# Kernel tuning notes

Measured on AMD Instinct MI355X. Metric: run time of the kernel, lower is better.

The kernel has to match this reference:

```python
import jax, jax.numpy as jnp
import numpy as np

B, D = 64, 11                 # trees, tree depth
T = 2 ** D - 1                # 2047 nodes per perfect binary tree (heap layout)
H, E, L, V = 256, 256, 5, 50000
LEAF_START = 2 ** (D - 1) - 1 # first leaf index within a tree
N = B * T


def setup_inputs() -> dict:
    key = jax.random.key(0)
    ks = jax.random.split(key, 8)
    wordid = jax.random.randint(ks[0], (N, L), 0, V, dtype=jnp.int32)
    # subtoken mask: 1 for leaf nodes (which carry tokens), 0 for internal nodes
    node_is_leaf = (jnp.arange(T) >= LEAF_START).astype(jnp.int32)      # [T]
    mask = jnp.tile(node_is_leaf[:, None], (B, L))                       # [N, L]
    h0 = jnp.zeros((N, H), jnp.float32)   # init_hidden -> zeros
    c0 = jnp.zeros((N, H), jnp.float32)
    list_root_index = jnp.zeros((B,), jnp.int32)          # root at offset 0 per tree
    list_num_node = jnp.full((B,), T, dtype=jnp.int32)
    s = 0.02
    emb_table = s * jax.random.normal(ks[1], (V, E), jnp.float32)
    W_iou = s * jax.random.normal(ks[2], (3 * H, E), jnp.float32)
    U_iou = s * jax.random.normal(ks[3], (3 * H, 2 * H), jnp.float32)
    b_iou = jnp.zeros((3 * H,), jnp.float32)
    U_f_w = s * jax.random.normal(ks[4], (2 * H, 2 * H), jnp.float32)
    U_f_b = jnp.zeros((2 * H,), jnp.float32)
    return {"wordid": wordid, "mask": mask, "h0": h0, "c0": c0,
            "list_root_index": list_root_index, "list_num_node": list_num_node,
            "emb_table": emb_table, "W_iou": W_iou, "U_iou": U_iou,
            "b_iou": b_iou, "U_f_w": U_f_w, "U_f_b": U_f_b}


def reference(wordid, mask, h0, c0, list_root_index, list_num_node,
              emb_table, W_iou, U_iou, b_iou, U_f_w, U_f_b):
    fm = mask.astype(jnp.float32)
    # tree_leaf_subtoken path: embed masked ids (masked slots hit token 0, as in torch)
    emb = emb_table[wordid * mask]                # [N, L, E]
    wemb = emb.sum(axis=1)                        # [N, E]
    leaf = fm.max(axis=1)                         # [N] node-level mask
    iou0 = (wemb @ W_iou.T) * leaf[:, None]       # [N, 3H] leaf input contribution
    iou0 = iou0.reshape(B, T, 3 * H)
    c0r = c0.reshape(B, T, H)

    def apply_node(iou, c_in):
        i, o, u = jnp.split(iou + b_iou, 3, axis=-1)
        cn = jax.nn.sigmoid(i) * jnp.tanh(u) + c_in
        return jax.nn.sigmoid(o) * jnp.tanh(cn), cn

    h = jnp.zeros((B, T, H), jnp.float32)
    c = jnp.zeros((B, T, H), jnp.float32)

    # frontier 0: leaves (no in-edges -> reduce never fires, c stays c0)
    hl, cl = apply_node(iou0[:, LEAF_START:], c0r[:, LEAF_START:])
    h = h.at[:, LEAF_START:].set(hl)
    c = c.at[:, LEAF_START:].set(cl)

    # topological propagation, level by level bottom-up
    for d in range(D - 2, -1, -1):
        s, e = 2 ** d - 1, 2 ** (d + 1) - 1
        n = e - s
        # children of nodes [s,e) are contiguous at [e, e+2n) as pairs (2i+1, 2i+2)
        h_cat = h[:, e:e + 2 * n].reshape(B, n, 2 * H)
        f = jax.nn.sigmoid(h_cat @ U_f_w.T + U_f_b).reshape(B, n, 2, H)
        c_red = (f * c[:, e:e + 2 * n].reshape(B, n, 2, H)).sum(axis=2)
        iou = h_cat @ U_iou.T                     # reduce_func REPLACES iou (DGL semantics)
        hn, cn = apply_node(iou, c_red)
        h = h.at[:, s:e].set(hn)
        c = c.at[:, s:e].set(cn)

    # all trees have T nodes -> padded tree_output is just h
    tree_output = h                               # [B, T, H]
    root_h, root_c = h[:, 0], c[:, 0]             # list_root_index == 0
    return tree_output, (root_h, root_c)
```

## Files before the change

### kernel.cpp

```cpp
#include <hip/hip_runtime.h>
#include <math.h>

typedef long long i64;
typedef short short8v __attribute__((ext_vector_type(8)));
typedef float float4v __attribute__((ext_vector_type(4)));

#define Hd 256
#define Bb 64
#define Tn 2047
#define LEAF0 1023
#define NTH 33538048LL

__device__ __forceinline__ float frcp(float x){ return __builtin_amdgcn_rcpf(x); }
__device__ __forceinline__ float sigm(float x){ return frcp(1.0f+__expf(-x)); }
__device__ __forceinline__ float ftanh(float x){ return 1.0f - 2.0f*frcp(__expf(2.0f*x)+1.0f); }
__device__ __forceinline__ float bf2f(unsigned short s){
  union { unsigned u; float f; } v; v.u = ((unsigned)s)<<16; return v.f; }
__device__ __forceinline__ short f2bf(float f){
  union { float f; unsigned u; } v; v.f = f;
  unsigned r = v.u + 0x7FFF + ((v.u>>16)&1);
  return (short)(r>>16); }

#define GL2LDS(gp, lp) __builtin_amdgcn_global_load_lds( \
  (const __attribute__((address_space(1))) void*)(gp), \
  (__attribute__((address_space(3))) void*)(lp), 16, 0, 0)

__global__ __launch_bounds__(256)
void wt2_kernel(const float* __restrict__ W_iou, const float* __restrict__ U_iou,
                const float* __restrict__ U_f_w,
                short* __restrict__ Wt2I, short* __restrict__ Wt2L){
  int t = blockIdx.x*256 + threadIdx.x;
  if (blockIdx.x < 320){
    int lane = t & 63, rest = t >> 6;
    int nr = rest % 20; int rest2 = rest / 20;
    int kt = rest2 & 15, hhb = rest2 >> 4;
    int g = nr/5, strip = nr - g*5;
    int j = strip*256 + hhb*64 + g*16 + (lane&15);
    int k0 = kt*32 + (lane>>4)*8;
    const float* src = (j < 768) ? (U_iou + (i64)j*512 + k0)
                                 : (U_f_w + (i64)(j-768)*512 + k0);
    short* dst = Wt2I + (i64)t*8;
    #pragma unroll
    for (int e=0;e<8;e++) dst[e] = f2bf(src[e]);
  } else {
    int t2 = t - 320*256;
    int lane = t2 & 63, rest = t2 >> 6;
    int nr = rest % 12; int rest2 = rest / 12;
    int kt = rest2 & 7, hhb = rest2 >> 3;
    int g = nr/3, strip = nr - g*3;
    int j = strip*256 + hhb*64 + g*16 + (lane&15);
    int k0 = kt*32 + (lane>>4)*8;
    const float* src = W_iou + (i64)j*256 + k0;
    short* dst = Wt2L + (i64)t2*8;
    #pragma unroll
    for (int e=0;e<8;e++) dst[e] = f2bf(src[e]);
  }
}

__global__ __launch_bounds__(256)
void wemb_kernel(const int* __restrict__ wordid, const float* __restrict__ emb,
                 short* __restrict__ hb, short* __restrict__ cbb){
  int id = blockIdx.x*256 + threadIdx.x;
  int row = id >> 5, q = id & 31;
  int b = row >> 10, j = row & 1023;
  i64 tb = (i64)b*Tn;
  const int* wid = wordid + (tb + LEAF0 + j)*5;
  float s[8];
  #pragma unroll
  for (int e=0;e<8;e++) s[e] = 0.f;
  #pragma unroll
  for (int l=0;l<5;l++){
    const float* er = emb + (i64)wid[l]*Hd + q*8;
    float4 v0 = *(const float4*)(er);
    float4 v1 = *(const float4*)(er+4);
    s[0]+=v0.x; s[1]+=v0.y; s[2]+=v0.z; s[3]+=v0.w;
    s[4]+=v1.x; s[5]+=v1.y; s[6]+=v1.z; s[7]+=v1.w;
  }
  short o[8];
  #pragma unroll
  for (int e=0;e<8;e++) o[e] = f2bf(s[e]);
  short* dst = (j < 1023) ? (hb + (tb + j)*Hd) : (cbb + tb*Hd);
  *(short8v*)(dst + q*8) = *(short8v*)o;
}

#define LEAF_ITER(KT, VM, BU, BL)                                            \
  {                                                                          \
    if ((KT)+2 < 8){                                                         \
      const short* bp = wbB + (i64)((KT)+2)*12*512;                          \
      _Pragma("unroll")                                                      \
      for (int s=0;s<3;s++) BL[s] = *(const short8v*)(bp + (i64)s*512);      \
    }                                                                        \
    asm volatile("" ::: "memory");                                           \
    if ((KT)+3 < 8) GL2LDS(srcA + ((KT)+3)*32, &As[((KT)+3)%5][w*512]);      \
    asm volatile("s_waitcnt vmcnt(" #VM ")" ::: "memory");                   \
    __builtin_amdgcn_s_barrier();                                            \
    asm volatile("" ::: "memory");                                           \
    short8v afr[4];                                                          \
    _Pragma("unroll")                                                        \
    for (int mr=0;mr<4;mr++)                                                 \
      afr[mr] = *(const short8v*)&As[(KT)%5][(wm*4+mr)*512 + lane*8];        \
    _Pragma("unroll")                                                        \
    for (int mr=0;mr<4;mr++)                                                 \
      _Pragma("unroll")                                                      \
      for (int s=0;s<3;s++)                                                  \
        acc[mr][s] = __builtin_amdgcn_mfma_f32_16x16x32_bf16(afr[mr], BU[s], acc[mr][s], 0, 0, 0); \
    asm volatile("s_waitcnt lgkmcnt(0)" ::: "memory");                       \
  }

__global__ __launch_bounds__(512)
void leaf_gemm(const short* __restrict__ hb, const short* __restrict__ cbb,
               const short* __restrict__ WB,
               const float* __restrict__ b_iou, const float* __restrict__ c0,
               float* __restrict__ hOut, short* __restrict__ hbOut,
               short* __restrict__ cbbOut){
  __shared__ __align__(16) short As[5][8*512];
  const int tid = threadIdx.x;
  const int lane = tid & 63, w = tid >> 6;
  const int wm = w >> 2, wg = w & 3;
  const int m0 = blockIdx.x*128;
  const int hhb = blockIdx.y;

  const int rA = m0 + w*16 + (lane&15);
  const int bA = rA >> 10, jA = rA & 1023;
  const short* baseA = (jA < 1023) ? (hb + ((i64)bA*Tn + jA)*Hd)
                                   : (cbb + (i64)bA*Tn*Hd);
  const short* srcA = baseA + (lane>>4)*8;
  const short* wbB = WB + (i64)hhb*96*512 + (i64)(wg*3)*512 + lane*8;

  float4v acc[4][3];
  #pragma unroll
  for (int mr=0;mr<4;mr++)
    #pragma unroll
    for (int s=0;s<3;s++){ float4v z = {0.f,0.f,0.f,0.f}; acc[mr][s] = z; }

  short8v b0[3], b1[3], b2[3];
  #pragma unroll
  for (int s=0;s<3;s++) b0[s] = *(const short8v*)(wbB + (i64)s*512);
  asm volatile("" ::: "memory");
  GL2LDS(srcA, &As[0][w*512]);
  GL2LDS(srcA + 32, &As[1][w*512]);
  GL2LDS(srcA + 64, &As[2][w*512]);
  asm volatile("" ::: "memory");
  #pragma unroll
  for (int s=0;s<3;s++) b1[s] = *(const short8v*)(wbB + (i64)(12+s)*512);
  asm volatile("" ::: "memory");

  LEAF_ITER(0,9,b0,b2)  LEAF_ITER(1,8,b1,b0)
  LEAF_ITER(2,9,b2,b1)  LEAF_ITER(3,9,b0,b2)
  LEAF_ITER(4,9,b1,b0)  LEAF_ITER(5,8,b2,b1)
  LEAF_ITER(6,4,b0,b2)  LEAF_ITER(7,0,b1,b0)

  const int hcol = hhb*64 + wg*16 + (lane&15);
  const float bi = b_iou[hcol], bo = b_iou[256+hcol], bu = b_iou[512+hcol];
  #pragma unroll
  for (int mr=0;mr<4;mr++){
    const int mgb = m0 + wm*64 + mr*16 + ((lane>>4)<<2);
    #pragma unroll
    for (int r=0;r<4;r++){
      const int m = mgb + r;
      const int b = m >> 10, j = m & 1023;
      const i64 n = (i64)b*Tn + LEAF0 + j;
      const float i_ = acc[mr][0][r] + bi;
      const float o_ = acc[mr][1][r] + bo;
      const float u_ = acc[mr][2][r] + bu;
      const float cn = sigm(i_)*ftanh(u_) + c0[n*Hd + hcol];
      const float hv = sigm(o_)*ftanh(cn);
      cbbOut[n*Hd + hcol] = f2bf(cn);
      hbOut[n*Hd + hcol]  = f2bf(hv);
      hOut[n*Hd + hcol] = hv;
    }
  }
}

#define LVL_ITER(KT, VM, BU, BL)                                             \
  {                                                                          \
    if ((KT)+2 < 16){                                                        \
      const short* bp = wbB + (i64)((KT)+2)*20*512;                          \
      _Pragma("unroll")                                                      \
      for (int s=0;s<5;s++) BL[s] = *(const short8v*)(bp + (i64)s*512);      \
    }                                                                        \
    asm volatile("" ::: "memory");                                           \
    if ((KT)+3 < 16) GL2LDS(srcA + ((KT)+3)*32, &As[((KT)+3)%5][w*512]);     \
    asm volatile("s_waitcnt vmcnt(" #VM ")" ::: "memory");                   \
    __builtin_amdgcn_s_barrier();                                            \
    asm volatile("" ::: "memory");                                           \
    short8v afr[4];                                                          \
    _Pragma("unroll")                                                        \
    for (int mr=0;mr<4;mr++)                                                 \
      afr[mr] = *(const short8v*)&As[(KT)%5][(wm*4+mr)*512 + lane*8];        \
    _Pragma("unroll")                                                        \
    for (int mr=0;mr<4;mr++)                                                 \
      _Pragma("unroll")                                                      \
      for (int s=0;s<5;s++)                                                  \
        acc[mr][s] = __builtin_amdgcn_mfma_f32_16x16x32_bf16(afr[mr], BU[s], acc[mr][s], 0, 0, 0); \
    asm volatile("s_waitcnt lgkmcnt(0)" ::: "memory");                       \
  }

__global__ __launch_bounds__(512)
void level_gemm(const short* __restrict__ WB,
                const float* __restrict__ b_iou, const float* __restrict__ U_f_b,
                float* __restrict__ hOut, short* __restrict__ hb, short* __restrict__ cbb,
                int s0, int e0, int logn){
  __shared__ __align__(16) short As[5][8*512];
  const int tid = threadIdx.x;
  const int lane = tid & 63, w = tid >> 6;
  const int wm = w >> 2, wg = w & 3;
  const int m0 = blockIdx.x*128;
  const int hhb = blockIdx.y;
  const int nm1 = (1<<logn)-1;

  const int rA = m0 + w*16 + (lane&15);
  const int bA = rA >> logn, jA = rA & nm1;
  const short* srcA = hb + ((i64)bA*Tn + e0)*Hd + (i64)jA*512 + (lane>>4)*8;
  const short* wbB = WB + (i64)hhb*320*512 + (i64)(wg*5)*512 + lane*8;

  float4v acc[4][5];
  #pragma unroll
  for (int mr=0;mr<4;mr++)
    #pragma unroll
    for (int s=0;s<5;s++){ float4v z = {0.f,0.f,0.f,0.f}; acc[mr][s] = z; }

  short8v b0[5], b1[5], b2[5];
  #pragma unroll
  for (int s=0;s<5;s++) b0[s] = *(const short8v*)(wbB + (i64)s*512);
  asm volatile("" ::: "memory");
  GL2LDS(srcA, &As[0][w*512]);
  GL2LDS(srcA + 32, &As[1][w*512]);
  GL2LDS(srcA + 64, &As[2][w*512]);
  asm volatile("" ::: "memory");
  #pragma unroll
  for (int s=0;s<5;s++) b1[s] = *(const short8v*)(wbB + (i64)(20+s)*512);
  asm volatile("" ::: "memory");

  LVL_ITER( 0,13,b0,b2)  LVL_ITER( 1,12,b1,b0)  LVL_ITER( 2,13,b2,b1)
  LVL_ITER( 3,13,b0,b2)  LVL_ITER( 4,13,b1,b0)  LVL_ITER( 5,13,b2,b1)
  LVL_ITER( 6,13,b0,b2)  LVL_ITER( 7,13,b1,b0)  LVL_ITER( 8,13,b2,b1)
  LVL_ITER( 9,13,b0,b2)  LVL_ITER(10,13,b1,b0)  LVL_ITER(11,13,b2,b1)
  LVL_ITER(12,13,b0,b2)  LVL_ITER(13,12,b1,b0)  LVL_ITER(14, 6,b2,b1)
  LVL_ITER(15, 0,b0,b2)

  const int hcol = hhb*64 + wg*16 + (lane&15);
  const float bi = b_iou[hcol], bo = b_iou[256+hcol], bu = b_iou[512+hcol];
  const float bfl = U_f_b[hcol], bfr2 = U_f_b[256+hcol];
  #pragma unroll
  for (int mr=0;mr<4;mr++){
    const int mgb = m0 + wm*64 + mr*16 + ((lane>>4)<<2);
    #pragma unroll
    for (int r=0;r<4;r++){
      const int m = mgb + r;
      const int b = m >> logn, j = m & nm1;
      const i64 base = (i64)b*Tn;
      const i64 cidx = (base + e0 + 2*j)*Hd + hcol;
      const float cl = bf2f((unsigned short)cbb[cidx]);
      const float cr = bf2f((unsigned short)cbb[cidx + Hd]);
      const float i_ = acc[mr][0][r]+bi, o_ = acc[mr][1][r]+bo, u_ = acc[mr][2][r]+bu;
      const float fl = acc[mr][3][r]+bfl, fr = acc[mr][4][r]+bfr2;
      const float cn = sigm(i_)*ftanh(u_) + sigm(fl)*cl + sigm(fr)*cr;
      const float hv = sigm(o_)*ftanh(cn);
      const i64 oidx = (base + s0 + j)*Hd + hcol;
      cbb[oidx] = f2bf(cn);
      hb[oidx]  = f2bf(hv);
      hOut[oidx] = hv;
    }
  }
}

__global__ __launch_bounds__(512)
void tree_fused(const short* __restrict__ WB, const float* __restrict__ b_iou,
                const float* __restrict__ U_f_b, float* __restrict__ hOut,
                const short* __restrict__ hb, const short* __restrict__ cbb,
                float* __restrict__ outRoot){
  __shared__ __align__(16) short BUF[192*256];
  short* L0H = BUF;
  short* L0C = BUF + 64*256;
  short* L1H = BUF + 128*256;
  short* L1C = BUF + 160*256;
  const int tid = threadIdx.x;
  const int lane = tid & 63, w = tid >> 6;
  const int wm = w >> 2, wg = w & 3;
  const int b = blockIdx.x;
  const i64 tb = (i64)b*Tn;

  #pragma unroll
  for (int p=0;p<4;p++){
    int idx = p*512 + tid;
    int row = idx >> 5, ch = idx & 31;
    int doff = ((row*256 + ch*8)*2) ^ ((row&7)<<4);
    short8v vh = *(const short8v*)(hb  + (tb + 63 + row)*Hd + ch*8);
    short8v vc = *(const short8v*)(cbb + (tb + 63 + row)*Hd + ch*8);
    *(short8v*)((char*)L0H + doff) = vh;
    *(short8v*)((char*)L0C + doff) = vc;
  }
  __syncthreads();

  short* inH = L0H; short* inC = L0C; short* outH = L1H; short* outC = L1C;

  for (int d = 5; d >= 0; --d){
    const int M = 1<<d, s0 = M-1;
    if (wm == 0 || d == 5){
      const int mg = (d == 5) ? wm*16 : 0;
      int j = mg + (lane&15); if (j > s0) j = s0;
      const int k0b = (lane>>4)*8;
      for (int hhb = 0; hhb < 4; ++hhb){
        float4v acc[5];
        #pragma unroll
        for (int s=0;s<5;s++){ float4v z = {0.f,0.f,0.f,0.f}; acc[s] = z; }
        const short* wbB = WB + (i64)hhb*320*512 + (i64)(wg*5)*512 + lane*8;
        #pragma unroll
        for (int kt=0; kt<16; ++kt){
          const int k0 = kt*32 + k0b;
          const int crow = 2*j + (k0>>8), ccol = k0 & 255;
          const int aoff = ((crow*256 + ccol)*2) ^ ((crow&7)<<4);
          short8v a = *(const short8v*)((const char*)inH + aoff);
          const short* bp = wbB + (i64)kt*20*512;
          #pragma unroll
          for (int s=0;s<5;s++){
            short8v bb = *(const short8v*)(bp + (i64)s*512);
            acc[s] = __builtin_amdgcn_mfma_f32_16x16x32_bf16(a, bb, acc[s], 0, 0, 0);
          }
        }
        const int hcol = hhb*64 + wg*16 + (lane&15);
        const float bi = b_iou[hcol], bo = b_iou[256+hcol], bu = b_iou[512+hcol];
        const float bfl = U_f_b[hcol], bfr2 = U_f_b[256+hcol];
        #pragma unroll
        for (int r=0;r<4;r++){
          const int row = mg + ((lane>>4)<<2) + r;
          if (row < M){
            const int c0r = 2*row, c1r = 2*row+1;
            const float cl = bf2f(*(const unsigned short*)((const char*)inC +
                              (((c0r*256 + hcol)*2) ^ ((c0r&7)<<4))));
            const float cr = bf2f(*(const unsigned short*)((const char*)inC +
                              (((c1r*256 + hcol)*2) ^ ((c1r&7)<<4))));
            const float i_ = acc[0][r]+bi, o_ = acc[1][r]+bo, u_ = acc[2][r]+bu;
            const float fl = acc[3][r]+bfl, fr = acc[4][r]+bfr2;
            const float cn = sigm(i_)*ftanh(u_) + sigm(fl)*cl + sigm(fr)*cr;
            const float hv = sigm(o_)*ftanh(cn);
            const int ooff = ((row*256 + hcol)*2) ^ ((row&7)<<4);
            *(short*)((char*)outH + ooff) = f2bf(hv);
            *(short*)((char*)outC + ooff) = f2bf(cn);
            hOut[(tb + s0 + row)*Hd + hcol] = hv;
            if (d == 0){
              outRoot[b*Hd + hcol] = hv;
              outRoot[Bb*Hd + b*Hd + hcol] = cn;
            }
          }
        }
      }
    }
    __syncthreads();
    short* t;
    t = inH; inH = outH; outH = t;
    t = inC; inC = outC; outC = t;
  }
}

extern "C" void kernel_launch(void* const* d_in, const int* in_sizes, int n_in,
                              void* d_out, int out_size, void* d_ws, size_t ws_size,
                              hipStream_t stream){
  const int*   wordid = (const int*)  d_in[0];
  const float* c0     = (const float*)d_in[3];
  const float* emb    = (const float*)d_in[6];
  const float* W_iou  = (const float*)d_in[7];
  const float* U_iou  = (const float*)d_in[8];
  const float* b_iou  = (const float*)d_in[9];
  const float* U_f_w  = (const float*)d_in[10];
  const float* U_f_b  = (const float*)d_in[11];

  float* hOut    = (float*)d_out;
  float* outRoot = hOut + NTH;
  short* cbb  = (short*)d_ws;
  short* hb   = cbb + NTH;
  short* Wt2I = hb + NTH;
  short* Wt2L = Wt2I + 655360;

  hipLaunchKernelGGL(wt2_kernel, dim3(416), dim3(256), 0, stream,
                     W_iou, U_iou, U_f_w, Wt2I, Wt2L);
  hipLaunchKernelGGL(wemb_kernel, dim3(8192), dim3(256), 0, stream,
                     wordid, emb, hb, cbb);
  hipLaunchKernelGGL(leaf_gemm, dim3(512,4), dim3(512), 0, stream,
                     hb, cbb, Wt2L, b_iou, c0, hOut, hb, cbb);
  for (int d = 9; d >= 6; --d){
    const int n = 1<<d, s = n-1, e = 2*n-1;
    const int bm = (64*n + 127)/128;
    hipLaunchKernelGGL(level_gemm, dim3(bm,4), dim3(512), 0, stream,
                       Wt2I, b_iou, U_f_b, hOut, hb, cbb, s, e, d);
  }
  hipLaunchKernelGGL(tree_fused, dim3(64), dim3(512), 0, stream,
                     Wt2I, b_iou, U_f_b, hOut, hb, cbb, outRoot);
}
```

Before: 400.5 us.

## Replace per-tree fused top-level kernel with per-level GEMM launches; merge prep kernels

Removes the tree_fused kernel, which ran the top six levels with one block per tree, and extends the level_gemm launch loop down to the root. level_gemm gains row clamping and bounds checks for levels smaller than a 128-row tile, and writes the root outputs when it processes the root level. The weight-conversion and embedding-sum kernels are merged into one prep kernel to save a launch. This spreads the small top levels over more CUs in exchange for six extra launches and round trips of h and c through global memory, where tree_fused kept them in LDS.

```diff
diff --git a/kernel.cpp b/kernel.cpp
--- a/kernel.cpp
+++ b/kernel.cpp
@@ -26,11 +26,13 @@
   (__attribute__((address_space(3))) void*)(lp), 16, 0, 0)
 
 __global__ __launch_bounds__(256)
-void wt2_kernel(const float* __restrict__ W_iou, const float* __restrict__ U_iou,
-                const float* __restrict__ U_f_w,
-                short* __restrict__ Wt2I, short* __restrict__ Wt2L){
-  int t = blockIdx.x*256 + threadIdx.x;
+void prep_kernel(const float* __restrict__ W_iou, const float* __restrict__ U_iou,
+                 const float* __restrict__ U_f_w,
+                 short* __restrict__ Wt2I, short* __restrict__ Wt2L,
+                 const int* __restrict__ wordid, const float* __restrict__ emb,
+                 short* __restrict__ hb, short* __restrict__ cbb){
   if (blockIdx.x < 320){
+    int t = blockIdx.x*256 + threadIdx.x;
     int lane = t & 63, rest = t >> 6;
     int nr = rest % 20; int rest2 = rest / 20;
     int kt = rest2 & 15, hhb = rest2 >> 4;
@@ -42,8 +44,8 @@
     short* dst = Wt2I + (i64)t*8;
     #pragma unroll
     for (int e=0;e<8;e++) dst[e] = f2bf(src[e]);
-  } else {
-    int t2 = t - 320*256;
+  } else if (blockIdx.x < 416){
+    int t2 = (blockIdx.x-320)*256 + threadIdx.x;
     int lane = t2 & 63, rest = t2 >> 6;
     int nr = rest % 12; int rest2 = rest / 12;
     int kt = rest2 & 7, hhb = rest2 >> 3;
@@ -54,33 +56,29 @@
     short* dst = Wt2L + (i64)t2*8;
     #pragma unroll
     for (int e=0;e<8;e++) dst[e] = f2bf(src[e]);
-  }
-}
-
-__global__ __launch_bounds__(256)
-void wemb_kernel(const int* __restrict__ wordid, const float* __restrict__ emb,
-                 short* __restrict__ hb, short* __restrict__ cbb){
-  int id = blockIdx.x*256 + threadIdx.x;
-  int row = id >> 5, q = id & 31;
-  int b = row >> 10, j = row & 1023;
-  i64 tb = (i64)b*Tn;
-  const int* wid = wordid + (tb + LEAF0 + j)*5;
-  float s[8];
-  #pragma unroll
-  for (int e=0;e<8;e++) s[e] = 0.f;
-  #pragma unroll
-  for (int l=0;l<5;l++){
-    const float* er = emb + (i64)wid[l]*Hd + q*8;
-    float4 v0 = *(const float4*)(er);
-    float4 v1 = *(const float4*)(er+4);
-    s[0]+=v0.x; s[1]+=v0.y; s[2]+=v0.z; s[3]+=v0.w;
-    s[4]+=v1.x; s[5]+=v1.y; s[6]+=v1.z; s[7]+=v1.w;
-  }
-  short o[8];
-  #pragma unroll
-  for (int e=0;e<8;e++) o[e] = f2bf(s[e]);
-  short* dst = (j < 1023) ? (hb + (tb + j)*Hd) : (cbb + tb*Hd);
-  *(short8v*)(dst + q*8) = *(short8v*)o;
+  } else {
+    int id = (blockIdx.x-416)*256 + threadIdx.x;
+    int row = id >> 5, q = id & 31;
+    int b = row >> 10, j = row & 1023;
+    i64 tb = (i64)b*Tn;
+    const int* wid = wordid + (tb + LEAF0 + j)*5;
+    float s[8];
+    #pragma unroll
+    for (int e=0;e<8;e++) s[e] = 0.f;
+    #pragma unroll
+    for (int l=0;l<5;l++){
+      const float* er = emb + (i64)wid[l]*Hd + q*8;
+      float4 v0 = *(const float4*)(er);
+      float4 v1 = *(const float4*)(er+4);
+      s[0]+=v0.x; s[1]+=v0.y; s[2]+=v0.z; s[3]+=v0.w;
+      s[4]+=v1.x; s[5]+=v1.y; s[6]+=v1.z; s[7]+=v1.w;
+    }
+    short o[8];
+    #pragma unroll
+    for (int e=0;e<8;e++) o[e] = f2bf(s[e]);
+    short* dst = (j < 1023) ? (hb + (tb + j)*Hd) : (cbb + tb*Hd);
+    *(short8v*)(dst + q*8) = *(short8v*)o;
+  }
 }
 
 #define LEAF_ITER(KT, VM, BU, BL)                                            \
@@ -200,16 +198,17 @@
 void level_gemm(const short* __restrict__ WB,
                 const float* __restrict__ b_iou, const float* __restrict__ U_f_b,
                 float* __restrict__ hOut, short* __restrict__ hb, short* __restrict__ cbb,
-                int s0, int e0, int logn){
+                float* __restrict__ outRoot, int s0, int e0, int logn){
   __shared__ __align__(16) short As[5][8*512];
   const int tid = threadIdx.x;
   const int lane = tid & 63, w = tid >> 6;
   const int wm = w >> 2, wg = w & 3;
   const int m0 = blockIdx.x*128;
   const int hhb = blockIdx.y;
+  const int Mtot = Bb << logn;
   const int nm1 = (1<<logn)-1;
 
-  const int rA = m0 + w*16 + (lane&15);
+  int rA = m0 + w*16 + (lane&15); if (rA >= Mtot) rA = Mtot-1;
   const int bA = rA >> logn, jA = rA & nm1;
   const short* srcA = hb + ((i64)bA*Tn + e0)*Hd + (i64)jA*512 + (lane>>4)*8;
   const short* wbB = WB + (i64)hhb*320*512 + (i64)(wg*5)*512 + lane*8;
@@ -248,109 +247,26 @@
     #pragma unroll
     for (int r=0;r<4;r++){
       const int m = mgb + r;
-      const int b = m >> logn, j = m & nm1;
-      const i64 base = (i64)b*Tn;
-      const i64 cidx = (base + e0 + 2*j)*Hd + hcol;
-      const float cl = bf2f((unsigned short)cbb[cidx]);
-      const float cr = bf2f((unsigned short)cbb[cidx + Hd]);
-      const float i_ = acc[mr][0][r]+bi, o_ = acc[mr][1][r]+bo, u_ = acc[mr][2][r]+bu;
-      const float fl = acc[mr][3][r]+bfl, fr = acc[mr][4][r]+bfr2;
-      const float cn = sigm(i_)*ftanh(u_) + sigm(fl)*cl + sigm(fr)*cr;
-      const float hv = sigm(o_)*ftanh(cn);
-      const i64 oidx = (base + s0 + j)*Hd + hcol;
-      cbb[oidx] = f2bf(cn);
-      hb[oidx]  = f2bf(hv);
-      hOut[oidx] = hv;
-    }
-  }
-}
-
-__global__ __launch_bounds__(512)
-void tree_fused(const short* __restrict__ WB, const float* __restrict__ b_iou,
-                const float* __restrict__ U_f_b, float* __restrict__ hOut,
-                const short* __restrict__ hb, const short* __restrict__ cbb,
-                float* __restrict__ outRoot){
-  __shared__ __align__(16) short BUF[192*256];
-  short* L0H = BUF;
-  short* L0C = BUF + 64*256;
-  short* L1H = BUF + 128*256;
-  short* L1C = BUF + 160*256;
-  const int tid = threadIdx.x;
-  const int lane = tid & 63, w = tid >> 6;
-  const int wm = w >> 2, wg = w & 3;
-  const int b = blockIdx.x;
-  const i64 tb = (i64)b*Tn;
-
-  #pragma unroll
-  for (int p=0;p<4;p++){
-    int idx = p*512 + tid;
-    int row = idx >> 5, ch = idx & 31;
-    int doff = ((row*256 + ch*8)*2) ^ ((row&7)<<4);
-    short8v vh = *(const short8v*)(hb  + (tb + 63 + row)*Hd + ch*8);
-    short8v vc = *(const short8v*)(cbb + (tb + 63 + row)*Hd + ch*8);
-    *(short8v*)((char*)L0H + doff) = vh;
-    *(short8v*)((char*)L0C + doff) = vc;
-  }
-  __syncthreads();
-
-  short* inH = L0H; short* inC = L0C; short* outH = L1H; short* outC = L1C;
-
-  for (int d = 5; d >= 0; --d){
-    const int M = 1<<d, s0 = M-1;
-    if (wm == 0 || d == 5){
-      const int mg = (d == 5) ? wm*16 : 0;
-      int j = mg + (lane&15); if (j > s0) j = s0;
-      const int k0b = (lane>>4)*8;
-      for (int hhb = 0; hhb < 4; ++hhb){
-        float4v acc[5];
-        #pragma unroll
-        for (int s=0;s<5;s++){ float4v z = {0.f,0.f,0.f,0.f}; acc[s] = z; }
-        const short* wbB = WB + (i64)hhb*320*512 + (i64)(wg*5)*512 + lane*8;
-        #pragma unroll
-        for (int kt=0; kt<16; ++kt){
-          const int k0 = kt*32 + k0b;
-          const int crow = 2*j + (k0>>8), ccol = k0 & 255;
-          const int aoff = ((crow*256 + ccol)*2) ^ ((crow&7)<<4);
-          short8v a = *(const short8v*)((const char*)inH + aoff);
-          const short* bp = wbB + (i64)kt*20*512;
-          #pragma unroll
-          for (int s=0;s<5;s++){
-            short8v bb = *(const short8v*)(bp + (i64)s*512);
-            acc[s] = __builtin_amdgcn_mfma_f32_16x16x32_bf16(a, bb, acc[s], 0, 0, 0);
-          }
-        }
-        const int hcol = hhb*64 + wg*16 + (lane&15);
-        const float bi = b_iou[hcol], bo = b_iou[256+hcol], bu = b_iou[512+hcol];
-        const float bfl = U_f_b[hcol], bfr2 = U_f_b[256+hcol];
-        #pragma unroll
-        for (int r=0;r<4;r++){
-          const int row = mg + ((lane>>4)<<2) + r;
-          if (row < M){
-            const int c0r = 2*row, c1r = 2*row+1;
-            const float cl = bf2f(*(const unsigned short*)((const char*)inC +
-                              (((c0r*256 + hcol)*2) ^ ((c0r&7)<<4))));
-            const float cr = bf2f(*(const unsigned short*)((const char*)inC +
-                              (((c1r*256 + hcol)*2) ^ ((c1r&7)<<4))));
-            const float i_ = acc[0][r]+bi, o_ = acc[1][r]+bo, u_ = acc[2][r]+bu;
-            const float fl = acc[3][r]+bfl, fr = acc[4][r]+bfr2;
-            const float cn = sigm(i_)*ftanh(u_) + sigm(fl)*cl + sigm(fr)*cr;
-            const float hv = sigm(o_)*ftanh(cn);
-            const int ooff = ((row*256 + hcol)*2) ^ ((row&7)<<4);
-            *(short*)((char*)outH + ooff) = f2bf(hv);
-            *(short*)((char*)outC + ooff) = f2bf(cn);
-            hOut[(tb + s0 + row)*Hd + hcol] = hv;
-            if (d == 0){
-              outRoot[b*Hd + hcol] = hv;
-              outRoot[Bb*Hd + b*Hd + hcol] = cn;
-            }
-          }
+      if (m < Mtot){
+        const int b = m >> logn, j = m & nm1;
+        const i64 base = (i64)b*Tn;
+        const i64 cidx = (base + e0 + 2*j)*Hd + hcol;
+        const float cl = bf2f((unsigned short)cbb[cidx]);
+        const float cr = bf2f((unsigned short)cbb[cidx + Hd]);
+        const float i_ = acc[mr][0][r]+bi, o_ = acc[mr][1][r]+bo, u_ = acc[mr][2][r]+bu;
+        const float fl = acc[mr][3][r]+bfl, fr = acc[mr][4][r]+bfr2;
+        const float cn = sigm(i_)*ftanh(u_) + sigm(fl)*cl + sigm(fr)*cr;
+        const float hv = sigm(o_)*ftanh(cn);
+        const i64 oidx = (base + s0 + j)*Hd + hcol;
+        cbb[oidx] = f2bf(cn);
+        hb[oidx]  = f2bf(hv);
+        hOut[oidx] = hv;
+        if (s0 == 0){
+          outRoot[b*Hd + hcol] = hv;
+          outRoot[Bb*Hd + b*Hd + hcol] = cn;
         }
       }
     }
-    __syncthreads();
-    short* t;
-    t = inH; inH = outH; outH = t;
-    t = inC; inC = outC; outC = t;
   }
 }
 
@@ -373,18 +289,14 @@
   short* Wt2I = hb + NTH;
   short* Wt2L = Wt2I + 655360;
 
-  hipLaunchKernelGGL(wt2_kernel, dim3(416), dim3(256), 0, stream,
-                     W_iou, U_iou, U_f_w, Wt2I, Wt2L);
-  hipLaunchKernelGGL(wemb_kernel, dim3(8192), dim3(256), 0, stream,
-                     wordid, emb, hb, cbb);
+  hipLaunchKernelGGL(prep_kernel, dim3(8608), dim3(256), 0, stream,
+                     W_iou, U_iou, U_f_w, Wt2I, Wt2L, wordid, emb, hb, cbb);
   hipLaunchKernelGGL(leaf_gemm, dim3(512,4), dim3(512), 0, stream,
                      hb, cbb, Wt2L, b_iou, c0, hOut, hb, cbb);
-  for (int d = 9; d >= 6; --d){
+  for (int d = 9; d >= 0; --d){
     const int n = 1<<d, s = n-1, e = 2*n-1;
     const int bm = (64*n + 127)/128;
-    hipLaunchKernelGGL(level_gemm, dim3(bm,4), dim3(512), 0, stream,
-                       Wt2I, b_iou, U_f_b, hOut, hb, cbb, s, e, d);
-  }
-  hipLaunchKernelGGL(tree_fused, dim3(64), dim3(512), 0, stream,
-                     Wt2I, b_iou, U_f_b, hOut, hb, cbb, outRoot);
+    hipLaunchKernelGGL(level_gemm, dim3(bm < 1 ? 1 : bm, 4), dim3(512), 0, stream,
+                       Wt2I, b_iou, U_f_b, hOut, hb, cbb, outRoot, s, e, d);
+  }
 }
```

Result: slower. 420.4 us (+5.0%).
